# Performance work log

Hardware: AMD Instinct MI355X
Metric: run time of the kernel (lower is better)

Reference implementation:

```python
import jax, jax.numpy as jnp
import numpy as np

N, D, K = 20000, 64, 32
EPS = 1e-5


def _knn_numpy(coords, k):
    # exact KNN, chunked; self is nearest (distance 0) -> index 0 column
    n = coords.shape[0]
    sq = (coords ** 2).sum(1)
    out = np.empty((n, k), np.int64)
    for s in range(0, n, 2000):
        c = coords[s:s + 2000]
        d = sq[None, :] - 2.0 * c @ coords.T  # row-constant term dropped
        part = np.argpartition(d, k - 1, axis=1)[:, :k]
        dp = np.take_along_axis(d, part, 1)
        order = np.argsort(dp, axis=1)
        out[s:s + 2000] = np.take_along_axis(part, order, 1)
    return out


def setup_inputs() -> dict:
    key = jax.random.key(0)
    ks = jax.random.split(key, 24)
    coords = jax.random.uniform(ks[0], (N, 3), dtype=jnp.float32) * 100.0
    feats = jax.random.normal(ks[1], (N, D), dtype=jnp.float32)
    knn_idx = jnp.asarray(_knn_numpy(np.asarray(coords), K + 1))  # [N, 33], self first

    def lin(k, fi, fo):
        return jax.random.normal(k, (fi, fo), dtype=jnp.float32) / np.sqrt(fi).astype(np.float32)

    def vec(k, fo):
        return jax.random.normal(k, (fo,), dtype=jnp.float32) * 0.01

    return {
        'coords': coords, 'feats': feats,
        'Wq': lin(ks[2], D, D), 'bq': vec(ks[3], D),
        'Wk': lin(ks[4], D, D), 'bk': vec(ks[5], D),
        'Wv': lin(ks[6], D, D), 'bv': vec(ks[7], D),
        'Wl1': lin(ks[8], 3, D), 'bl1': vec(ks[9], D),
        'Wl2': lin(ks[10], D, D), 'bl2': vec(ks[11], D),
        'Ww1': lin(ks[12], D, D), 'bw1': vec(ks[13], D),
        'Ww2': lin(ks[14], D, D), 'bw2': vec(ks[15], D),
        'g_att': jnp.ones((D,), jnp.float32), 'b_att': jnp.zeros((D,), jnp.float32),
        'Wsg': lin(ks[16], D + 3, D), 'bsg': vec(ks[17], D),
        'Wf': lin(ks[18], D, D), 'bf': vec(ks[19], D),
        'g_ff': jnp.ones((D,), jnp.float32), 'b_ff': jnp.zeros((D,), jnp.float32),
        'knn_idx': knn_idx,
    }


def _sparsemax_axis1(z):
    # sparsemax over axis=1 of [n, k, d] (matches torch Sparsemax(dim=1))
    zt = jnp.moveaxis(z, 1, -1)  # [n, d, k]
    z_sorted = jnp.flip(jnp.sort(zt, axis=-1), axis=-1)
    csum = jnp.cumsum(z_sorted, axis=-1)
    r = jnp.arange(1, zt.shape[-1] + 1, dtype=zt.dtype)
    support = 1.0 + r * z_sorted > csum
    k_sup = jnp.sum(support, axis=-1, keepdims=True)  # int, >=1
    tau = (jnp.take_along_axis(csum, k_sup - 1, axis=-1) - 1.0) / k_sup.astype(zt.dtype)
    return jnp.moveaxis(jnp.maximum(zt - tau, 0.0), -1, 1)


def _layernorm(x, g, b):
    m = jnp.mean(x, -1, keepdims=True)
    v = jnp.mean((x - m) ** 2, -1, keepdims=True)
    return g * (x - m) * jax.lax.rsqrt(v + EPS) + b


def reference(coords, feats, Wq, bq, Wk, bk, Wv, bv, Wl1, bl1, Wl2, bl2,
              Ww1, bw1, Ww2, bw2, g_att, b_att, Wsg, bsg, Wf, bf, g_ff, b_ff,
              knn_idx):
    n = feats.shape[0]
    # ---- RNSA (knn_points includes self: first K columns) ----
    idx = knn_idx[:, :K]                                   # [N, K]
    diff = coords[idx] - coords[:, None, :]                # [N, K, 3]
    fc = jax.nn.relu(diff @ Wl1 + bl1) @ Wl2 + bl2         # positional MLP [N, K, D]
    pe = fc + feats[idx]                                   # positional embedding
    Q = jax.nn.relu(feats @ Wq + bq)                       # [N, D]
    Kf = jax.nn.relu(pe @ Wk + bk)                         # [N, K, D]
    V = pe @ Wv + bv                                       # [N, K, D]
    rel = (Kf - Q[:, None, :]) * fc
    w = jax.nn.relu(rel @ Ww1 + bw1) @ Ww2 + bw2
    w = _sparsemax_axis1(w)                                # dropout: eval mode -> identity
    attn = jnp.einsum('nkd,nkd->nd', V, w)
    x_att = feats + attn                                   # RNSA residual (x + attended)
    x_att = x_att + feats                                  # outer residual in GraphFormer

    # ---- feed-forward: LayerNorm + SGConv(K=1) + linear + residual + LayerNorm ----
    h = _layernorm(x_att, g_att, b_att)
    x_in = jnp.concatenate([h, coords], axis=-1)           # [N, D+3]
    # knn_graph(loop=False): 32 nearest excluding self -> columns 1..32
    src = knn_idx[:, 1:K + 1].reshape(-1)
    dst = jnp.repeat(jnp.arange(n), K)
    self_idx = jnp.arange(n)
    src_all = jnp.concatenate([src, self_idx])             # gcn_norm adds self loops
    dst_all = jnp.concatenate([dst, self_idx])
    deg = jax.ops.segment_sum(jnp.ones_like(src_all, dtype=x_in.dtype), dst_all, num_segments=n)
    norm = jax.lax.rsqrt(deg[src_all] * deg[dst_all])
    agg = jax.ops.segment_sum(x_in[src_all] * norm[:, None], dst_all, num_segments=n)
    x_ff = agg @ Wsg + bsg
    x_ff = jax.nn.relu(x_ff)
    x_ff = x_ff @ Wf + bf                                  # dropout: eval -> identity
    x_out = x_ff + h
    return _layernorm(x_out, g_ff, b_ff)
```

## Files before the change

kernel.cpp:

```cpp
#include <hip/hip_runtime.h>

#define NPTS 20000
#define EPSF 1e-5f

typedef _Float16 half8 __attribute__((ext_vector_type(8)));
typedef float floatx4 __attribute__((ext_vector_type(4)));

__device__ __forceinline__ half8 ldWt(const _Float16* __restrict__ w,
                                      int c15, int g, int nt, int ks) {
  int c = nt * 16 + c15;
  int kg = ks * 4 + g;
  return *(const half8*)(w + c * 64 + ((kg ^ (c & 7)) << 3));
}

__device__ __forceinline__ half8 ldWtF32(const float* __restrict__ W,
                                         int c15, int g, int nt, int ks) {
  int c = nt * 16 + c15;
  half8 r;
#pragma unroll
  for (int j = 0; j < 8; ++j) r[j] = (_Float16)W[(ks * 32 + g * 8 + j) * 64 + c];
  return r;
}

__device__ __forceinline__ void stC(float* __restrict__ Tw, int c15, int g,
                                    int mt, int nt, floatx4 v) {
  int col = nt * 16 + c15;
  int chunk = mt * 4 + g;
  *(floatx4*)(Tw + col * 32 + ((chunk ^ (col & 7)) << 2)) = v;
}

__device__ __forceinline__ floatx4 ldCread(const float* __restrict__ Tw,
                                           int c15, int g, int mt, int nt) {
  int col = nt * 16 + c15;
  int chunk = mt * 4 + g;
  return *(const floatx4*)(Tw + col * 32 + ((chunk ^ (col & 7)) << 2));
}

__device__ __forceinline__ half8 ldA(const float* __restrict__ Tw,
                                     int c15, int g, int mt, int ks) {
  int m = mt * 16 + c15;
  half8 r;
#pragma unroll
  for (int j = 0; j < 8; ++j) {
    int c = ks * 32 + g * 8 + j;
    r[j] = (_Float16)Tw[c * 32 + (((m >> 2) ^ j) << 2) + (m & 3)];
  }
  return r;
}

__device__ __forceinline__ void ldAfrags(const float* __restrict__ Tw,
                                         int c15, int g, half8 a[2][2]) {
#pragma unroll
  for (int mt = 0; mt < 2; ++mt)
#pragma unroll
    for (int ks = 0; ks < 2; ++ks) a[mt][ks] = ldA(Tw, c15, g, mt, ks);
}

__device__ __forceinline__ void domm(const _Float16* __restrict__ w,
                                     const half8 a[2][2], int c15, int g,
                                     floatx4 acc[2][4]) {
#pragma unroll
  for (int ks = 0; ks < 2; ++ks)
#pragma unroll
    for (int nt = 0; nt < 4; ++nt) {
      half8 b = ldWt(w, c15, g, nt, ks);
#pragma unroll
      for (int mt = 0; mt < 2; ++mt)
        acc[mt][nt] = __builtin_amdgcn_mfma_f32_16x16x32_f16(a[mt][ks], b, acc[mt][nt], 0, 0, 0);
    }
}

__device__ __forceinline__ void domm1(const _Float16* __restrict__ w,
                                      const half8 a[2], int c15, int g,
                                      floatx4 acc[4]) {
#pragma unroll
  for (int ks = 0; ks < 2; ++ks)
#pragma unroll
    for (int nt = 0; nt < 4; ++nt) {
      half8 b = ldWt(w, c15, g, nt, ks);
      acc[nt] = __builtin_amdgcn_mfma_f32_16x16x32_f16(a[ks], b, acc[nt], 0, 0, 0);
    }
}

__global__ __launch_bounds__(256) void prep_q_kernel(
    const float* __restrict__ Wl2, const float* __restrict__ Wv,
    const float* __restrict__ Wk, const float* __restrict__ Ww1,
    const float* __restrict__ Ww2, const float* __restrict__ Wsg,
    const float* __restrict__ Wf, const float* __restrict__ Wq,
    const float* __restrict__ feats, const float* __restrict__ bq,
    _Float16* __restrict__ wtg, _Float16* __restrict__ Qh)
{
  if (blockIdx.x < 7) {
    const float* srcs[7] = {Wl2, Wv, Wk, Ww1, Ww2, Wsg, Wf};
    const float* src = srcs[blockIdx.x];
    _Float16* dst = wtg + blockIdx.x * 4096;
    int t = threadIdx.x;
#pragma unroll
    for (int i = 0; i < 16; ++i) {
      int lin = i * 256 + t;
      int k = lin >> 6, d = lin & 63;
      dst[d * 64 + (((k >> 3) ^ (d & 7)) << 3) + (k & 7)] = (_Float16)src[lin];
    }
    return;
  }
  const int wv = threadIdx.x >> 6, lane = threadIdx.x & 63;
  const int c15 = lane & 15, g = lane >> 4;
  const int n0 = ((blockIdx.x - 7) * 4 + wv) * 32;

  half8 a[2][2];
#pragma unroll
  for (int mt = 0; mt < 2; ++mt) {
    int r = n0 + mt * 16 + c15;
    if (r > NPTS - 1) r = NPTS - 1;
#pragma unroll
    for (int ks = 0; ks < 2; ++ks) {
      const float* p = feats + (size_t)r * 64 + ks * 32 + g * 8;
      float4 u0 = *(const float4*)p, u1 = *(const float4*)(p + 4);
      a[mt][ks][0] = (_Float16)u0.x; a[mt][ks][1] = (_Float16)u0.y;
      a[mt][ks][2] = (_Float16)u0.z; a[mt][ks][3] = (_Float16)u0.w;
      a[mt][ks][4] = (_Float16)u1.x; a[mt][ks][5] = (_Float16)u1.y;
      a[mt][ks][6] = (_Float16)u1.z; a[mt][ks][7] = (_Float16)u1.w;
    }
  }
  floatx4 acc[2][4] = {};
#pragma unroll
  for (int ks = 0; ks < 2; ++ks)
#pragma unroll
    for (int nt = 0; nt < 4; ++nt) {
      half8 b = ldWtF32(Wq, c15, g, nt, ks);
#pragma unroll
      for (int mt = 0; mt < 2; ++mt)
        acc[mt][nt] = __builtin_amdgcn_mfma_f32_16x16x32_f16(a[mt][ks], b, acc[mt][nt], 0, 0, 0);
    }
#pragma unroll
  for (int nt = 0; nt < 4; ++nt) {
    float bqv = bq[nt * 16 + c15];
#pragma unroll
    for (int mt = 0; mt < 2; ++mt)
#pragma unroll
      for (int r = 0; r < 4; ++r) {
        int n = n0 + mt * 16 + g * 4 + r;
        if (n < NPTS)
          Qh[(size_t)n * 64 + nt * 16 + c15] = (_Float16)fmaxf(acc[mt][nt][r] + bqv, 0.f);
      }
  }
}

__global__ __launch_bounds__(256, 4) void attn_kernel(
    const float* __restrict__ coords, const float* __restrict__ feats,
    const float* __restrict__ bk, const float* __restrict__ bv,
    const float* __restrict__ Wl1, const float* __restrict__ bl1,
    const float* __restrict__ bl2, const float* __restrict__ bw1,
    const float* __restrict__ bw2, const float* __restrict__ g_att,
    const float* __restrict__ b_att, const int* __restrict__ knn,
    const _Float16* __restrict__ wtg, const _Float16* __restrict__ Qh,
    _Float16* __restrict__ h_out)
{
  __shared__ float Tsh[4][2048];
  const int wv = threadIdx.x >> 6, lane = threadIdx.x & 63;
  const int c15 = lane & 15, g = lane >> 4;
  const int n = blockIdx.x * 4 + wv;
  float* Tw = Tsh[wv];
  const int* row = knn + (size_t)n * 33;

  const _Float16* wt_l2 = wtg;
  const _Float16* wt_v  = wtg + 4096;
  const _Float16* wt_k  = wtg + 8192;
  const _Float16* wt_w1 = wtg + 12288;
  const _Float16* wt_w2 = wtg + 16384;

  half8 aH[2][2];
  {
    float cnx = coords[(size_t)n * 3], cny = coords[(size_t)n * 3 + 1],
          cnz = coords[(size_t)n * 3 + 2];
#pragma unroll
    for (int ks = 0; ks < 2; ++ks) {
      int c0 = ks * 32 + g * 8;
      float4 wx0 = *(const float4*)(Wl1 + c0),       wx1 = *(const float4*)(Wl1 + c0 + 4);
      float4 wy0 = *(const float4*)(Wl1 + 64 + c0),  wy1 = *(const float4*)(Wl1 + 64 + c0 + 4);
      float4 wz0 = *(const float4*)(Wl1 + 128 + c0), wz1 = *(const float4*)(Wl1 + 128 + c0 + 4);
      float4 bb0 = *(const float4*)(bl1 + c0),       bb1 = *(const float4*)(bl1 + c0 + 4);
      float wx[8] = {wx0.x,wx0.y,wx0.z,wx0.w,wx1.x,wx1.y,wx1.z,wx1.w};
      float wy[8] = {wy0.x,wy0.y,wy0.z,wy0.w,wy1.x,wy1.y,wy1.z,wy1.w};
      float wz[8] = {wz0.x,wz0.y,wz0.z,wz0.w,wz1.x,wz1.y,wz1.z,wz1.w};
      float bb[8] = {bb0.x,bb0.y,bb0.z,bb0.w,bb1.x,bb1.y,bb1.z,bb1.w};
#pragma unroll
      for (int mt = 0; mt < 2; ++mt) {
        int id = row[mt * 16 + c15];
        float dx = coords[(size_t)id * 3] - cnx;
        float dy = coords[(size_t)id * 3 + 1] - cny;
        float dz = coords[(size_t)id * 3 + 2] - cnz;
#pragma unroll
        for (int j = 0; j < 8; ++j)
          aH[mt][ks][j] = (_Float16)fmaxf(dx * wx[j] + dy * wy[j] + dz * wz[j] + bb[j], 0.f);
      }
    }
  }

  {
    floatx4 fcacc[2][4] = {};
    domm(wt_l2, aH, c15, g, fcacc);
#pragma unroll
    for (int nt = 0; nt < 4; ++nt) {
      float b = bl2[nt * 16 + c15];
#pragma unroll
      for (int mt = 0; mt < 2; ++mt) stC(Tw, c15, g, mt, nt, fcacc[mt][nt] + b);
    }
  }
  __builtin_amdgcn_wave_barrier();

  half8 aP[2][2];
#pragma unroll
  for (int mt = 0; mt < 2; ++mt) {
    int m = mt * 16 + c15;
    int rn = row[m];
#pragma unroll
    for (int ks = 0; ks < 2; ++ks) {
      const float* fp = feats + (size_t)rn * 64 + ks * 32 + g * 8;
      float4 u0 = *(const float4*)fp, u1 = *(const float4*)(fp + 4);
      float fv[8] = {u0.x,u0.y,u0.z,u0.w,u1.x,u1.y,u1.z,u1.w};
#pragma unroll
      for (int j = 0; j < 8; ++j) {
        int c = ks * 32 + g * 8 + j;
        float fcv = Tw[c * 32 + (((m >> 2) ^ j) << 2) + (m & 3)];
        aP[mt][ks][j] = (_Float16)(fcv + fv[j]);
      }
    }
  }
  __builtin_amdgcn_wave_barrier();

  {
    floatx4 KR[2][4] = {};
    domm(wt_k, aP, c15, g, KR);
    __builtin_amdgcn_wave_barrier();
#pragma unroll
    for (int nt = 0; nt < 4; ++nt) {
      float bkv = bk[nt * 16 + c15];
      float q4 = (float)Qh[(size_t)n * 64 + nt * 16 + c15];
#pragma unroll
      for (int mt = 0; mt < 2; ++mt) {
        floatx4 fcq = ldCread(Tw, c15, g, mt, nt);
        floatx4 v;
#pragma unroll
        for (int r = 0; r < 4; ++r)
          v[r] = (fmaxf(KR[mt][nt][r] + bkv, 0.f) - q4) * fcq[r];
        stC(Tw, c15, g, mt, nt, v);
      }
    }
  }
  __builtin_amdgcn_wave_barrier();
  half8 aR[2][2];
  ldAfrags(Tw, c15, g, aR);

  {
    floatx4 W1[2][4] = {};
    domm(wt_w1, aR, c15, g, W1);
    __builtin_amdgcn_wave_barrier();
#pragma unroll
    for (int nt = 0; nt < 4; ++nt) {
      float b = bw1[nt * 16 + c15];
#pragma unroll
      for (int mt = 0; mt < 2; ++mt) {
        floatx4 v;
#pragma unroll
        for (int r = 0; r < 4; ++r) v[r] = fmaxf(W1[mt][nt][r] + b, 0.f);
        stC(Tw, c15, g, mt, nt, v);
      }
    }
  }
  __builtin_amdgcn_wave_barrier();
  half8 aW[2][2];
  ldAfrags(Tw, c15, g, aW);

  {
    floatx4 WW[2][4] = {};
    domm(wt_w2, aW, c15, g, WW);
    __builtin_amdgcn_wave_barrier();
#pragma unroll
    for (int nt = 0; nt < 4; ++nt) {
      float b = bw2[nt * 16 + c15];
#pragma unroll
      for (int mt = 0; mt < 2; ++mt) stC(Tw, c15, g, mt, nt, WW[mt][nt] + b);
    }
  }
  __builtin_amdgcn_wave_barrier();

  float tau;
  {
    float a[32];
#pragma unroll
    for (int i = 0; i < 8; ++i) {
      floatx4 ch = *(const floatx4*)(Tw + lane * 32 + ((i ^ (lane & 7)) << 2));
#pragma unroll
      for (int r = 0; r < 4; ++r) a[i * 4 + r] = ch[r];
    }
#pragma unroll
    for (int size = 2; size <= 32; size <<= 1) {
#pragma unroll
      for (int stride = size >> 1; stride > 0; stride >>= 1) {
#pragma unroll
        for (int i = 0; i < 32; ++i) {
          int j = i ^ stride;
          if (j > i) {
            float x = a[i], y = a[j];
            float lo = fminf(x, y), hi = fmaxf(x, y);
            bool up = ((i & size) == 0);
            a[i] = up ? hi : lo;
            a[j] = up ? lo : hi;
          }
        }
      }
    }
    float csum = 0.f, csel = 0.f;
    int ksup = 1;
#pragma unroll
    for (int i = 0; i < 32; ++i) {
      csum += a[i];
      if (1.0f + (float)(i + 1) * a[i] > csum) { ksup = i + 1; csel = csum; }
    }
    tau = (csel - 1.0f) / (float)ksup;
  }

  floatx4 V[2][4] = {};
  domm(wt_v, aP, c15, g, V);
#pragma unroll
  for (int nt = 0; nt < 4; ++nt) {
    float b = bv[nt * 16 + c15];
#pragma unroll
    for (int mt = 0; mt < 2; ++mt) V[mt][nt] += b;
  }

  float x4[4];
#pragma unroll
  for (int nt = 0; nt < 4; ++nt) {
    float t4 = __shfl(tau, nt * 16 + c15, 64);
    float ssum = 0.f;
#pragma unroll
    for (int mt = 0; mt < 2; ++mt) {
      floatx4 w4 = ldCread(Tw, c15, g, mt, nt);
#pragma unroll
      for (int r = 0; r < 4; ++r)
        ssum += fmaxf(w4[r] - t4, 0.f) * V[mt][nt][r];
    }
    ssum += __shfl_xor(ssum, 16, 64);
    ssum += __shfl_xor(ssum, 32, 64);
    x4[nt] = 2.f * feats[(size_t)n * 64 + nt * 16 + c15] + ssum;
  }

  float sum = x4[0] + x4[1] + x4[2] + x4[3];
  float sum2 = x4[0] * x4[0] + x4[1] * x4[1] + x4[2] * x4[2] + x4[3] * x4[3];
#pragma unroll
  for (int m = 1; m < 16; m <<= 1) {
    sum += __shfl_xor(sum, m, 64);
    sum2 += __shfl_xor(sum2, m, 64);
  }
  float mean = sum * (1.f / 64.f);
  float var = sum2 * (1.f / 64.f) - mean * mean;
  float inv = rsqrtf(var + EPSF);
  h_out[(size_t)n * 64 + lane] =
      (_Float16)(g_att[lane] * (x4[g] - mean) * inv + b_att[lane]);
}

__global__ __launch_bounds__(256) void gconv_kernel(
    const float* __restrict__ coords, const _Float16* __restrict__ h,
    const _Float16* __restrict__ wtg, const float* __restrict__ Wsg,
    const float* __restrict__ bsg, const float* __restrict__ bf,
    const float* __restrict__ g_ff, const float* __restrict__ b_ff,
    const int* __restrict__ knn, float* __restrict__ out)
{
  __shared__ float Tsh[4][2048];
  const int wv = threadIdx.x >> 6, lane = threadIdx.x & 63;
  const int c15 = lane & 15, g = lane >> 4;
  const int n0 = (blockIdx.x * 4 + wv) * 16;
  if (n0 >= NPTS) return;
  float* Tw = Tsh[wv];
  const _Float16* wt_sg = wtg + 5 * 4096;
  const _Float16* wt_f  = wtg + 6 * 4096;
  const float inv33 = 1.0f / 33.0f;

  const int p = n0 + c15;
  const int* row = knn + (size_t)p * 33;
  float acc0[8] = {}, acc1[8] = {};
#pragma unroll 11
  for (int k = 0; k < 33; ++k) {
    int idx = (k == 0) ? p : row[k];
    const _Float16* hp = h + (size_t)idx * 64 + g * 8;
    half8 v0 = *(const half8*)hp;
    half8 v1 = *(const half8*)(hp + 32);
#pragma unroll
    for (int j = 0; j < 8; ++j) {
      acc0[j] += (float)v0[j];
      acc1[j] += (float)v1[j];
    }
  }
  float sx = 0.f, sy = 0.f, sz = 0.f;
  for (int k = g; k < 33; k += 4) {
    int idx = (k == 0) ? p : row[k];
    sx += coords[(size_t)idx * 3];
    sy += coords[(size_t)idx * 3 + 1];
    sz += coords[(size_t)idx * 3 + 2];
  }
  sx += __shfl_xor(sx, 16, 64); sx += __shfl_xor(sx, 32, 64);
  sy += __shfl_xor(sy, 16, 64); sy += __shfl_xor(sy, 32, 64);
  sz += __shfl_xor(sz, 16, 64); sz += __shfl_xor(sz, 32, 64);
  float cxa = sx * inv33, cya = sy * inv33, cza = sz * inv33;

  half8 aA[2];
#pragma unroll
  for (int j = 0; j < 8; ++j) {
    aA[0][j] = (_Float16)(acc0[j] * inv33);
    aA[1][j] = (_Float16)(acc1[j] * inv33);
  }

  {
    floatx4 C1[4] = {};
    domm1(wt_sg, aA, c15, g, C1);
#pragma unroll
    for (int nt = 0; nt < 4; ++nt) {
      int col = nt * 16 + c15;
      float b = bsg[col];
      float w64 = Wsg[4096 + col], w65 = Wsg[4160 + col], w66 = Wsg[4224 + col];
      floatx4 v;
#pragma unroll
      for (int r = 0; r < 4; ++r) {
        int src = g * 4 + r;
        float cx = __shfl(cxa, src, 64);
        float cy = __shfl(cya, src, 64);
        float cz = __shfl(cza, src, 64);
        v[r] = fmaxf(C1[nt][r] + b + cx * w64 + cy * w65 + cz * w66, 0.f);
      }
      stC(Tw, c15, g, 0, nt, v);
    }
  }
  __builtin_amdgcn_wave_barrier();
  half8 aT[2];
  aT[0] = ldA(Tw, c15, g, 0, 0);
  aT[1] = ldA(Tw, c15, g, 0, 1);

  floatx4 C2[4] = {};
  domm1(wt_f, aT, c15, g, C2);
#pragma unroll
  for (int nt = 0; nt < 4; ++nt) {
    float b = bf[nt * 16 + c15];
#pragma unroll
    for (int r = 0; r < 4; ++r)
      C2[nt][r] += b + (float)h[(size_t)(n0 + g * 4 + r) * 64 + nt * 16 + c15];
  }
#pragma unroll
  for (int r = 0; r < 4; ++r) {
    float s = C2[0][r] + C2[1][r] + C2[2][r] + C2[3][r];
    float s2 = C2[0][r] * C2[0][r] + C2[1][r] * C2[1][r] +
               C2[2][r] * C2[2][r] + C2[3][r] * C2[3][r];
#pragma unroll
    for (int m = 1; m < 16; m <<= 1) {
      s += __shfl_xor(s, m, 64);
      s2 += __shfl_xor(s2, m, 64);
    }
    float mean = s * (1.f / 64.f);
    float var = s2 * (1.f / 64.f) - mean * mean;
    float inv = rsqrtf(var + EPSF);
    int prow = n0 + g * 4 + r;
#pragma unroll
    for (int nt = 0; nt < 4; ++nt) {
      int col = nt * 16 + c15;
      out[(size_t)prow * 64 + col] =
          g_ff[col] * (C2[nt][r] - mean) * inv + b_ff[col];
    }
  }
}

extern "C" void kernel_launch(void* const* d_in, const int* in_sizes, int n_in,
                              void* d_out, int out_size, void* d_ws, size_t ws_size,
                              hipStream_t stream) {
  (void)in_sizes; (void)n_in; (void)out_size; (void)ws_size;
  const float* coords = (const float*)d_in[0];
  const float* feats  = (const float*)d_in[1];
  const float* Wq  = (const float*)d_in[2];  const float* bq  = (const float*)d_in[3];
  const float* Wk  = (const float*)d_in[4];  const float* bk  = (const float*)d_in[5];
  const float* Wv  = (const float*)d_in[6];  const float* bv  = (const float*)d_in[7];
  const float* Wl1 = (const float*)d_in[8];  const float* bl1 = (const float*)d_in[9];
  const float* Wl2 = (const float*)d_in[10]; const float* bl2 = (const float*)d_in[11];
  const float* Ww1 = (const float*)d_in[12]; const float* bw1 = (const float*)d_in[13];
  const float* Ww2 = (const float*)d_in[14]; const float* bw2 = (const float*)d_in[15];
  const float* g_att = (const float*)d_in[16]; const float* b_att = (const float*)d_in[17];
  const float* Wsg = (const float*)d_in[18]; const float* bsg = (const float*)d_in[19];
  const float* Wf  = (const float*)d_in[20]; const float* bf  = (const float*)d_in[21];
  const float* g_ff = (const float*)d_in[22]; const float* b_ff = (const float*)d_in[23];
  const int* knn = (const int*)d_in[24];

  _Float16* h   = (_Float16*)d_ws;
  _Float16* wtg = (_Float16*)((char*)d_ws + 2621440);
  _Float16* Qh  = (_Float16*)((char*)d_ws + 2621440 + 57344);
  float* out = (float*)d_out;

  prep_q_kernel<<<dim3(164), dim3(256), 0, stream>>>(
      Wl2, Wv, Wk, Ww1, Ww2, Wsg, Wf, Wq, feats, bq, wtg, Qh);
  attn_kernel<<<dim3(NPTS / 4), dim3(256), 0, stream>>>(
      coords, feats, bk, bv, Wl1, bl1, bl2, bw1, bw2,
      g_att, b_att, knn, wtg, Qh, h);
  gconv_kernel<<<dim3(313), dim3(256), 0, stream>>>(
      coords, h, wtg, Wsg, bsg, bf, g_ff, b_ff, knn, out);
}
```

Baseline: 218.8 us.

## Spread gconv neighbor gathering across all four waves per 16-point tile

The graph-conv kernel now assigns 16 points per block instead of 64. All four waves gather neighbor features, one point at a time with one lane per channel, and stage the means in shared memory. Wave 0 alone then runs both small MFMA matmuls and the LayerNorm. This launches about four times as many blocks to raise parallelism in the latency-bound gather. The cost is a block-wide sync and three idle waves during the matmul phase.

```diff
diff --git a/kernel.cpp b/kernel.cpp
--- a/kernel.cpp
+++ b/kernel.cpp
@@ -368,48 +368,69 @@
     const float* __restrict__ g_ff, const float* __restrict__ b_ff,
     const int* __restrict__ knn, float* __restrict__ out)
 {
-  __shared__ float Tsh[4][2048];
+  __shared__ float agg_s[16 * 68];
+  __shared__ float cm_s[16 * 4];
+  __shared__ float T2[2048];
   const int wv = threadIdx.x >> 6, lane = threadIdx.x & 63;
   const int c15 = lane & 15, g = lane >> 4;
-  const int n0 = (blockIdx.x * 4 + wv) * 16;
-  if (n0 >= NPTS) return;
-  float* Tw = Tsh[wv];
+  const int n0 = blockIdx.x * 16;
+  const float inv33 = 1.0f / 33.0f;
   const _Float16* wt_sg = wtg + 5 * 4096;
   const _Float16* wt_f  = wtg + 6 * 4096;
-  const float inv33 = 1.0f / 33.0f;
-
-  const int p = n0 + c15;
-  const int* row = knn + (size_t)p * 33;
-  float acc0[8] = {}, acc1[8] = {};
-#pragma unroll 11
-  for (int k = 0; k < 33; ++k) {
-    int idx = (k == 0) ? p : row[k];
-    const _Float16* hp = h + (size_t)idx * 64 + g * 8;
-    half8 v0 = *(const half8*)hp;
-    half8 v1 = *(const half8*)(hp + 32);
-#pragma unroll
-    for (int j = 0; j < 8; ++j) {
-      acc0[j] += (float)v0[j];
-      acc1[j] += (float)v1[j];
-    }
-  }
-  float sx = 0.f, sy = 0.f, sz = 0.f;
-  for (int k = g; k < 33; k += 4) {
-    int idx = (k == 0) ? p : row[k];
-    sx += coords[(size_t)idx * 3];
-    sy += coords[(size_t)idx * 3 + 1];
-    sz += coords[(size_t)idx * 3 + 2];
-  }
-  sx += __shfl_xor(sx, 16, 64); sx += __shfl_xor(sx, 32, 64);
-  sy += __shfl_xor(sy, 16, 64); sy += __shfl_xor(sy, 32, 64);
-  sz += __shfl_xor(sz, 16, 64); sz += __shfl_xor(sz, 32, 64);
-  float cxa = sx * inv33, cya = sy * inv33, cza = sz * inv33;
+
+#pragma unroll
+  for (int i = 0; i < 4; ++i) {
+    int pl = wv * 4 + i;
+    int p = n0 + pl;
+    int idxv = 0;
+    if (lane < 33) idxv = knn[(size_t)p * 33 + lane];
+    float acc = (float)h[(size_t)p * 64 + lane];
+#pragma unroll 8
+    for (int k = 1; k <= 32; ++k) {
+      int idx = __shfl(idxv, k, 64);
+      acc += (float)h[(size_t)idx * 64 + lane];
+    }
+    agg_s[pl * 68 + lane] = acc * inv33;
+    float sx = 0.f, sy = 0.f, sz = 0.f;
+    if (lane < 33) {
+      int src = (lane == 0) ? p : idxv;
+      sx = coords[(size_t)src * 3];
+      sy = coords[(size_t)src * 3 + 1];
+      sz = coords[(size_t)src * 3 + 2];
+    }
+#pragma unroll
+    for (int m = 1; m < 64; m <<= 1) {
+      sx += __shfl_xor(sx, m, 64);
+      sy += __shfl_xor(sy, m, 64);
+      sz += __shfl_xor(sz, m, 64);
+    }
+    if (lane == 0) {
+      cm_s[pl * 4 + 0] = sx * inv33;
+      cm_s[pl * 4 + 1] = sy * inv33;
+      cm_s[pl * 4 + 2] = sz * inv33;
+    }
+  }
+  __syncthreads();
+  if (wv != 0) return;
 
   half8 aA[2];
 #pragma unroll
-  for (int j = 0; j < 8; ++j) {
-    aA[0][j] = (_Float16)(acc0[j] * inv33);
-    aA[1][j] = (_Float16)(acc1[j] * inv33);
+  for (int ks = 0; ks < 2; ++ks) {
+    const float* pr = agg_s + c15 * 68 + ks * 32 + g * 8;
+    float4 u0 = *(const float4*)pr, u1 = *(const float4*)(pr + 4);
+    aA[ks][0] = (_Float16)u0.x; aA[ks][1] = (_Float16)u0.y;
+    aA[ks][2] = (_Float16)u0.z; aA[ks][3] = (_Float16)u0.w;
+    aA[ks][4] = (_Float16)u1.x; aA[ks][5] = (_Float16)u1.y;
+    aA[ks][6] = (_Float16)u1.z; aA[ks][7] = (_Float16)u1.w;
+  }
+
+  float cmx[4], cmy[4], cmz[4];
+#pragma unroll
+  for (int r = 0; r < 4; ++r) {
+    int pl = g * 4 + r;
+    cmx[r] = cm_s[pl * 4 + 0];
+    cmy[r] = cm_s[pl * 4 + 1];
+    cmz[r] = cm_s[pl * 4 + 2];
   }
 
   {
@@ -422,29 +443,25 @@
       float w64 = Wsg[4096 + col], w65 = Wsg[4160 + col], w66 = Wsg[4224 + col];
       floatx4 v;
 #pragma unroll
-      for (int r = 0; r < 4; ++r) {
-        int src = g * 4 + r;
-        float cx = __shfl(cxa, src, 64);
-        float cy = __shfl(cya, src, 64);
-        float cz = __shfl(cza, src, 64);
-        v[r] = fmaxf(C1[nt][r] + b + cx * w64 + cy * w65 + cz * w66, 0.f);
-      }
-      stC(Tw, c15, g, 0, nt, v);
+      for (int r = 0; r < 4; ++r)
+        v[r] = fmaxf(C1[nt][r] + b + cmx[r] * w64 + cmy[r] * w65 + cmz[r] * w66, 0.f);
+      stC(T2, c15, g, 0, nt, v);
     }
   }
   __builtin_amdgcn_wave_barrier();
   half8 aT[2];
-  aT[0] = ldA(Tw, c15, g, 0, 0);
-  aT[1] = ldA(Tw, c15, g, 0, 1);
+  aT[0] = ldA(T2, c15, g, 0, 0);
+  aT[1] = ldA(T2, c15, g, 0, 1);
 
   floatx4 C2[4] = {};
   domm1(wt_f, aT, c15, g, C2);
 #pragma unroll
   for (int nt = 0; nt < 4; ++nt) {
-    float b = bf[nt * 16 + c15];
+    int col = nt * 16 + c15;
+    float b = bf[col];
 #pragma unroll
     for (int r = 0; r < 4; ++r)
-      C2[nt][r] += b + (float)h[(size_t)(n0 + g * 4 + r) * 64 + nt * 16 + c15];
+      C2[nt][r] += b + (float)h[(size_t)(n0 + g * 4 + r) * 64 + col];
   }
 #pragma unroll
   for (int r = 0; r < 4; ++r) {
@@ -498,6 +515,6 @@
   attn_kernel<<<dim3(NPTS / 4), dim3(256), 0, stream>>>(
       coords, feats, bk, bv, Wl1, bl1, bl2, bw1, bw2,
       g_att, b_att, knn, wtg, Qh, h);
-  gconv_kernel<<<dim3(313), dim3(256), 0, stream>>>(
+  gconv_kernel<<<dim3(NPTS / 16), dim3(256), 0, stream>>>(
       coords, h, wtg, Wsg, bsg, bf, g_ff, b_ff, knn, out);
 }
```

Measured after the change: 212.5 us. -2.9%, faster.
